# Kernel tuning notes

Measured on AMD Instinct MI355X. Metric: run time of the kernel, lower is better.

Reference implementation:

```python
import jax, jax.numpy as jnp
import numpy as np

B, S, D = 2048, 8, 1280
K = 1                 # n_components_remove
HIGH_T = 0.6          # PC1_HIGH_ACTIVITY_THRESHOLD
STORM_T = 0.8         # solar_storm_threshold


def setup_inputs() -> dict:
    key = jax.random.key(0)
    k1, k2 = jax.random.split(key, 2)
    features = jax.random.normal(k1, (B, S, D), dtype=jnp.float32)
    kp_index = jax.random.uniform(k2, (B,), dtype=jnp.float32) * 9.0
    cmr_gate = jnp.ones((1,), dtype=jnp.float32)  # nn.Parameter(torch.ones(1))
    return {"features": features, "kp_index": kp_index, "cmr_gate": cmr_gate}


def reference(features, kp_index, cmr_gate):
    # Per-sample standardization over the feature axis (numpy std, ddof=0)
    mu = features.mean(axis=2, keepdims=True)            # (B, S, 1)
    sigma = features.std(axis=2, keepdims=True) + 1e-8   # (B, S, 1)
    fn = (features - mu) / sigma                         # (B, S, D)

    # Batched thin SVD of the (S, D) normalized feature matrix
    U, sv, Vt = jnp.linalg.svd(fn, full_matrices=False)  # (B,S,S), (B,S), (B,S,D)
    var = sv * sv
    pc1_ratio = var[:, 0] / (var.sum(axis=-1) + 1e-8)    # (B,)

    # solar_flag: 0 normal, 1 high activity, 2 storm
    solar_flag = (pc1_ratio >= HIGH_T).astype(jnp.int32) + (pc1_ratio >= STORM_T).astype(jnp.int32)

    # Rank-K reconstruction of the common-mode (solar) component
    low = jnp.einsum('bsk,bk,bkd->bsd', U[:, :, :K], sv[:, :K], Vt[:, :K, :])
    clean = (fn - low) * sigma + mu                      # de-normalized cleaned features

    # Kp-gating: amplify CMR when Kp >= 5
    kp_gate = 1.0 + 0.5 * (kp_index >= 5.0).astype(features.dtype)[:, None, None]
    clean = features + kp_gate * (clean - features)

    # Learnable gate
    gate = jax.nn.sigmoid(cmr_gate)[0]
    features_clean = features + gate * (clean - features)
    return features_clean, pc1_ratio, solar_flag
```

## Files before the change

### kernel.cpp

```cpp
#include <hip/hip_runtime.h>
#include <math.h>


#define SV 8
#define DV 1280
#define D4 320
#define BSTRIDE (SV*DV)
#define LDW 44
#define WSS 17

__global__ __launch_bounds__(320)
void cmr_stats(const float* __restrict__ feat,
               const float* __restrict__ kp,
               const float* __restrict__ cmr_gate,
               float* __restrict__ cws,
               float* __restrict__ out,
               int Bn)
{
    __shared__ float lds[44 * LDW];
    const int tid  = threadIdx.x;
    const int lane = tid & 63;
    const int wq   = tid >> 6;
    const int b    = blockIdx.x;

    const float4* __restrict__ f4 = (const float4*)(feat + (size_t)b * BSTRIDE);
    const int d4 = wq * 64 + lane;
    float4 f[8];
#pragma unroll
    for (int s = 0; s < 8; ++s) f[s] = f4[s * D4 + d4];

    float Sr[8], C[36];
#pragma unroll
    for (int s = 0; s < 8; ++s) Sr[s] = (f[s].x + f[s].y) + (f[s].z + f[s].w);
    {
        int idx = 0;
#pragma unroll
        for (int i2 = 0; i2 < 8; ++i2)
#pragma unroll
            for (int j2 = i2; j2 < 8; ++j2) {
                float t0 = fmaf(f[i2].x, f[j2].x, fmaf(f[i2].y, f[j2].y, 0.f));
                C[idx] = fmaf(f[i2].z, f[j2].z, fmaf(f[i2].w, f[j2].w, t0));
                ++idx;
            }
    }
#pragma unroll
    for (int m = 1; m <= 4; m <<= 1) {
#pragma unroll
        for (int s = 0; s < 8; ++s) Sr[s] += __shfl_xor(Sr[s], m);
#pragma unroll
        for (int t = 0; t < 36; ++t) C[t] += __shfl_xor(C[t], m);
    }
    {
        const int p = wq * 8 + (lane >> 3);
        if ((lane & 7) == 0) {
#pragma unroll
            for (int t = 0; t < 36; ++t) lds[t * LDW + p] = C[t];
#pragma unroll
            for (int s = 0; s < 8; ++s) lds[(36 + s) * LDW + p] = Sr[s];
        }
    }
    __syncthreads();
    if (wq != 0) return;

    float tot;
    {
        const float4* l4 = (const float4*)lds;
        const int Lr = (lane < 44) ? lane : 0;
        float4 a4 = make_float4(0.f, 0.f, 0.f, 0.f);
#pragma unroll
        for (int q = 0; q < 10; ++q) {
            float4 v = l4[Lr * (LDW / 4) + q];
            a4.x += v.x; a4.y += v.y; a4.z += v.z; a4.w += v.w;
        }
        tot = (a4.x + a4.y) + (a4.z + a4.w);
    }

    const int i = lane >> 3, j = lane & 7;
    const int a_ = (i < j) ? i : j;
    const int b_ = (i < j) ? j : i;
    const int tii = 8 * i - (i * (i - 1)) / 2;
    const int tjj = 8 * j - (j * (j - 1)) / 2;
    const int tij = 8 * a_ - (a_ * (a_ - 1)) / 2 + (b_ - a_);
    const float Cij = __shfl(tot, tij);
    const float Ci  = __shfl(tot, tii);
    const float Cj  = __shfl(tot, tjj);
    const float Si  = __shfl(tot, 36 + i);
    const float Sj  = __shfl(tot, 36 + j);

    const float invD = 1.f / (float)DV;
    const float mui = Si * invD, muj = Sj * invD;
    const float vari = fmaxf(Ci * invD - mui * mui, 0.f);
    const float varj = fmaxf(Cj * invD - muj * muj, 0.f);
    const float sigi  = sqrtf(vari) + 1e-8f;
    const float rsigi = 1.f / sigi;
    const float rsigj = 1.f / (sqrtf(varj) + 1e-8f);
    const float G = ((Cij - (float)DV * mui * muj) * rsigi) * rsigj;

    float tr = 0.f;
#pragma unroll
    for (int k = 0; k < 8; ++k) tr += __shfl(G, 9 * k);

    float A = G / fmaxf(tr, 1e-30f);
#pragma unroll
    for (int t = 0; t < 14; ++t) {
        float nb = 0.f;
#pragma unroll
        for (int k = 0; k < 8; ++k)
            nb = fmaf(__shfl(A, i * 8 + k), __shfl(A, k * 8 + j), nb);
        float dg = 0.f;
#pragma unroll
        for (int k = 0; k < 8; ++k) dg += __shfl(nb, 9 * k);
        A = nb / fmaxf(dg, 1e-30f);
    }
    float best = __shfl(A, 0); int bj = 0;
#pragma unroll
    for (int k = 1; k < 8; ++k) {
        float dk = __shfl(A, 9 * k);
        if (dk > best) { best = dk; bj = k; }
    }
    float u = __shfl(A, i * 8 + bj);
    {
        float nn = 0.f;
#pragma unroll
        for (int k = 0; k < 8; ++k) nn += __shfl(u * u, 9 * k);
        u *= rsqrtf(fmaxf(nn, 1e-30f));
    }
#pragma unroll
    for (int it = 0; it < 2; ++it) {
        float y = G * __shfl(u, 9 * j);
#pragma unroll
        for (int m = 1; m <= 4; m <<= 1) y += __shfl_xor(y, m);
        float ny = 0.f;
#pragma unroll
        for (int k = 0; k < 8; ++k) ny += __shfl(y * y, 9 * k);
        u = y * rsqrtf(fmaxf(ny, 1e-30f));
    }
    float v = G * u * __shfl(u, 9 * j);
#pragma unroll
    for (int m = 1; m <= 4; m <<= 1) v += __shfl_xor(v, m);
    float lam = 0.f;
#pragma unroll
    for (int k = 0; k < 8; ++k) lam += __shfl(v, 9 * k);
    const float pc1 = lam / (tr + 1e-8f);

    const float gate = 1.f / (1.f + expf(-cmr_gate[0]));
    const float kpg  = (kp[b] >= 5.0f) ? 1.5f : 1.0f;
    const float Gt   = gate * kpg;

    float bc = 0.f;
#pragma unroll
    for (int k = 0; k < 8; ++k) bc += __shfl(u * rsigi * mui, 9 * k);

    float* wsb = cws + (size_t)b * WSS;
    if (j == 0) {
        wsb[i]     = u * rsigi;
        wsb[8 + i] = Gt * sigi * u;
    }
    if (lane == 0) {
        wsb[16] = bc;
        out[(size_t)Bn * BSTRIDE + b] = pc1;
        const float flag = (pc1 >= 0.6f ? 1.f : 0.f) + (pc1 >= 0.8f ? 1.f : 0.f);
        out[(size_t)Bn * BSTRIDE + Bn + b] = flag;
    }
}

__global__ __launch_bounds__(320)
void cmr_apply(const float* __restrict__ feat,
               const float* __restrict__ cws,
               float* __restrict__ out)
{
    const int tid  = threadIdx.x;
    const int lane = tid & 63;
    const int wq   = tid >> 6;
    const int b    = blockIdx.x;

    const float* __restrict__ wsb = cws + (size_t)b * WSS;
    float a[8], c[8];
#pragma unroll
    for (int s = 0; s < 8; ++s) { a[s] = wsb[s]; c[s] = wsb[8 + s]; }
    const float bc = wsb[16];

    const float4* __restrict__ f4 = (const float4*)(feat + (size_t)b * BSTRIDE);
    float4* __restrict__ o4 = (float4*)(out + (size_t)b * BSTRIDE);
    const int d4 = wq * 64 + lane;

    float4 f[8];
#pragma unroll
    for (int s = 0; s < 8; ++s) f[s] = f4[s * D4 + d4];

    float4 p = make_float4(-bc, -bc, -bc, -bc);
#pragma unroll
    for (int s = 0; s < 8; ++s) {
        p.x = fmaf(a[s], f[s].x, p.x);
        p.y = fmaf(a[s], f[s].y, p.y);
        p.z = fmaf(a[s], f[s].z, p.z);
        p.w = fmaf(a[s], f[s].w, p.w);
    }
#pragma unroll
    for (int s = 0; s < 8; ++s) {
        float4 o;
        o.x = fmaf(-c[s], p.x, f[s].x);
        o.y = fmaf(-c[s], p.y, f[s].y);
        o.z = fmaf(-c[s], p.z, f[s].z);
        o.w = fmaf(-c[s], p.w, f[s].w);
        o4[s * D4 + d4] = o;
    }
}

extern "C" void kernel_launch(void* const* d_in, const int* in_sizes, int n_in,
                              void* d_out, int out_size, void* d_ws, size_t ws_size,
                              hipStream_t stream) {
    const float* feat = (const float*)d_in[0];
    const float* kp   = (const float*)d_in[1];
    const float* gate = (const float*)d_in[2];
    float* out = (float*)d_out;
    float* cws = (float*)d_ws;
    const int Bn = in_sizes[0] / BSTRIDE;

    cmr_stats<<<Bn, 320, 0, stream>>>(feat, kp, gate, cws, out, Bn);
    cmr_apply<<<Bn, 320, 0, stream>>>(feat, cws, out);
}
```

Before: 177.1 us.

## Split stats kernel into Gram reduction and batched per-wave eigen solve

The single stats kernel is split into two. The first computes per-sample Gram/sum statistics and writes 44 floats per sample to workspace. A new eigen kernel then runs the serial power-iteration solve with four samples per 256-thread block, one wave per sample. Before, each 320-thread block left four of its five waves idle while the lone wave did the long shuffle-heavy eigen loop, which held CU slots. The cost is one extra kernel launch and a small workspace round trip. Bn is assumed divisible by 4.

```diff
diff --git a/kernel.cpp b/kernel.cpp
--- a/kernel.cpp
+++ b/kernel.cpp
@@ -7,17 +7,14 @@
 #define D4 320
 #define BSTRIDE (SV*DV)
 #define LDW 44
+#define NP 44
 #define WSS 17
 
 __global__ __launch_bounds__(320)
-void cmr_stats(const float* __restrict__ feat,
-               const float* __restrict__ kp,
-               const float* __restrict__ cmr_gate,
-               float* __restrict__ cws,
-               float* __restrict__ out,
-               int Bn)
+void cmr_gram(const float* __restrict__ feat,
+              float* __restrict__ gram)
 {
-    __shared__ float lds[44 * LDW];
+    __shared__ float lds[NP * LDW];
     const int tid  = threadIdx.x;
     const int lane = tid & 63;
     const int wq   = tid >> 6;
@@ -62,18 +59,31 @@
     __syncthreads();
     if (wq != 0) return;
 
-    float tot;
-    {
+    if (lane < NP) {
         const float4* l4 = (const float4*)lds;
-        const int Lr = (lane < 44) ? lane : 0;
         float4 a4 = make_float4(0.f, 0.f, 0.f, 0.f);
 #pragma unroll
         for (int q = 0; q < 10; ++q) {
-            float4 v = l4[Lr * (LDW / 4) + q];
+            float4 v = l4[lane * (LDW / 4) + q];
             a4.x += v.x; a4.y += v.y; a4.z += v.z; a4.w += v.w;
         }
-        tot = (a4.x + a4.y) + (a4.z + a4.w);
-    }
+        gram[(size_t)b * NP + lane] = (a4.x + a4.y) + (a4.z + a4.w);
+    }
+}
+
+__global__ __launch_bounds__(256)
+void cmr_eigen(const float* __restrict__ gram,
+               const float* __restrict__ kp,
+               const float* __restrict__ cmr_gate,
+               float* __restrict__ coef,
+               float* __restrict__ out,
+               int Bn)
+{
+    const int lane = threadIdx.x & 63;
+    const int b = blockIdx.x * 4 + (threadIdx.x >> 6);
+
+    const int Lr = (lane < NP) ? lane : 0;
+    const float tot = gram[(size_t)b * NP + Lr];
 
     const int i = lane >> 3, j = lane & 7;
     const int a_ = (i < j) ? i : j;
@@ -151,7 +161,7 @@
 #pragma unroll
     for (int k = 0; k < 8; ++k) bc += __shfl(u * rsigi * mui, 9 * k);
 
-    float* wsb = cws + (size_t)b * WSS;
+    float* wsb = coef + (size_t)b * WSS;
     if (j == 0) {
         wsb[i]     = u * rsigi;
         wsb[8 + i] = Gt * sigi * u;
@@ -166,7 +176,7 @@
 
 __global__ __launch_bounds__(320)
 void cmr_apply(const float* __restrict__ feat,
-               const float* __restrict__ cws,
+               const float* __restrict__ coef,
                float* __restrict__ out)
 {
     const int tid  = threadIdx.x;
@@ -174,7 +184,7 @@
     const int wq   = tid >> 6;
     const int b    = blockIdx.x;
 
-    const float* __restrict__ wsb = cws + (size_t)b * WSS;
+    const float* __restrict__ wsb = coef + (size_t)b * WSS;
     float a[8], c[8];
 #pragma unroll
     for (int s = 0; s < 8; ++s) { a[s] = wsb[s]; c[s] = wsb[8 + s]; }
@@ -214,9 +224,12 @@
     const float* kp   = (const float*)d_in[1];
     const float* gate = (const float*)d_in[2];
     float* out = (float*)d_out;
-    float* cws = (float*)d_ws;
     const int Bn = in_sizes[0] / BSTRIDE;
 
-    cmr_stats<<<Bn, 320, 0, stream>>>(feat, kp, gate, cws, out, Bn);
-    cmr_apply<<<Bn, 320, 0, stream>>>(feat, cws, out);
-}
+    float* gram = (float*)d_ws;
+    float* coef = gram + (size_t)Bn * NP;
+
+    cmr_gram <<<Bn,      320, 0, stream>>>(feat, gram);
+    cmr_eigen<<<Bn / 4,  256, 0, stream>>>(gram, kp, gate, coef, out, Bn);
+    cmr_apply<<<Bn,      320, 0, stream>>>(feat, coef, out);
+}
```

Result: no change. 178.5 us (+0.8%).
